# Kernel optimization log

Measured on AMD Instinct MI355X. Metric: run time of the kernel, lower is better.

## Reference

```python
import jax, jax.numpy as jnp
import numpy as np

B, S, N, E = 8, 64, 512, 32  # batch, seq_size, node_num, embed_size


def setup_inputs() -> dict:
    key = jax.random.key(0)
    k0, k1, k2, k3, k4 = jax.random.split(key, 5)
    x = jax.random.normal(k0, (B, S, N), dtype=jnp.float32)
    # lin_w: Linear(2*S, E) -> weight (E, 2*S), bias (E,)
    W = jax.random.normal(k1, (E, 2 * S), dtype=jnp.float32) * (1.0 / np.sqrt(2 * S))
    b_w = jax.random.normal(k2, (E,), dtype=jnp.float32) * 0.01
    # lin_a: Linear(E, 1) -> weight (E,), bias scalar
    Wa = jax.random.normal(k3, (E,), dtype=jnp.float32) * (1.0 / np.sqrt(E))
    b_a = jax.random.normal(k4, (), dtype=jnp.float32) * 0.01
    return {"x": x, "W": W, "b_w": b_w, "Wa": Wa, "b_a": b_a}


def reference(x, W, b_w, Wa, b_a):
    # Faithful to MP_GAT.forward in eval mode (dropout = identity).
    # Algebraic decomposition: lin_w(cat(vi, vj)) = vi @ Wi^T + vj @ Wj^T + b,
    # where W = [Wi | Wj] along the input dim -- avoids the O(N^2 * 2S) concat.
    s = W.shape[1] // 2
    v = jnp.transpose(x, (0, 2, 1))          # (B, N, S)
    Wi, Wj = W[:, :s], W[:, s:]              # (E, S) each
    ti = jnp.einsum('bns,es->bne', v, Wi)    # (B, N, E)
    tj = jnp.einsum('bns,es->bne', v, Wj)    # (B, N, E)
    pre = ti[:, :, None, :] + tj[:, None, :, :] + b_w  # (B, N, N, E)
    xw = jnp.where(pre > 0, pre, 0.2 * pre)  # LeakyReLU(0.2)
    e = jnp.einsum('bije,e->bij', xw, Wa) + b_a        # (B, N, N) = lin_a(...).squeeze
    attention = jax.nn.softmax(e, axis=2)
    h = jax.nn.sigmoid(jnp.einsum('bij,bjs->bis', attention, v))  # (B, N, S)
    return jnp.transpose(h, (0, 2, 1)), attention      # (B, S, N), (B, N, N)
```

## Files before the change

kernel.cpp:

```cpp
#include <hip/hip_runtime.h>
#include <math.h>

#define BB 8
#define SS 64
#define NN 512
#define EE 32
#define IT 16

typedef __attribute__((ext_vector_type(8))) short short8v;
typedef __attribute__((ext_vector_type(4))) float f32x4;

__device__ __forceinline__ unsigned short f2bf(float f) {
    union { float f; unsigned u; } v; v.f = f;
    unsigned r = v.u + 0x7fffu + ((v.u >> 16) & 1u);
    return (unsigned short)(r >> 16);
}
__device__ __forceinline__ float bflo(unsigned u) { return __uint_as_float(u << 16); }
__device__ __forceinline__ float bfhi(unsigned u) { return __uint_as_float(u & 0xffff0000u); }
__device__ __forceinline__ unsigned packtr(float lo, float hi) {
    return (__float_as_uint(hi) & 0xffff0000u) | (__float_as_uint(lo) >> 16);
}

__global__ __launch_bounds__(128) void proj_kernel(
    const float* __restrict__ x, const float* __restrict__ W,
    const float* __restrict__ b_w, const float* __restrict__ Wa,
    float* __restrict__ tip, unsigned short* __restrict__ tjb,
    float* __restrict__ cip, float* __restrict__ djp)
{
    __shared__ float sW[SS][65];
    const int t = threadIdx.x;
    const int wg = ((blockIdx.x & 7) << 6) | (blockIdx.x >> 3);
    const int b = wg >> 6;
    const int n0 = (wg & 63) << 3;

#pragma unroll
    for (int r = 0; r < 8; ++r) {
        int idx = r * 512 + t * 4;
        float4 w4 = *(const float4*)(W + idx);
        int e = idx >> 7;
        int sp = idx & 127;
        int eo = ((sp >> 6) << 5) | e;
        int s0 = sp & 63;
        sW[s0 + 0][eo] = w4.x;
        sW[s0 + 1][eo] = w4.y;
        sW[s0 + 2][eo] = w4.z;
        sW[s0 + 3][eo] = w4.w;
    }
    __syncthreads();

    const int eo = t & 63;
    const int ng = t >> 6;
    const float* xb = x + (size_t)b * SS * NN + n0 + (ng << 2);
    float a0 = 0.f, a1 = 0.f, a2 = 0.f, a3 = 0.f;
#pragma unroll 8
    for (int s = 0; s < SS; ++s) {
        float wv = sW[s][eo];
        float4 xv = *(const float4*)(xb + (size_t)s * NN);
        a0 = fmaf(wv, xv.x, a0);
        a1 = fmaf(wv, xv.y, a1);
        a2 = fmaf(wv, xv.z, a2);
        a3 = fmaf(wv, xv.w, a3);
    }
    const int e = eo & 31;
    const bool isI = eo < EE;
    if (isI) {
        float bias = b_w[e];
        a0 += bias; a1 += bias; a2 += bias; a3 += bias;
        *(float4*)(tip + ((size_t)(b * EE + e)) * NN + n0 + (ng << 2)) =
            make_float4(a0, a1, a2, a3);
    } else {
        unsigned u0 = f2bf(a0) | ((unsigned)f2bf(a1) << 16);
        unsigned u1 = f2bf(a2) | ((unsigned)f2bf(a3) << 16);
        *(uint2*)(tjb + ((size_t)(b * EE + e)) * NN + n0 + (ng << 2)) =
            make_uint2(u0, u1);
    }

    float wa = Wa[e];
    float r0 = wa * a0, r1 = wa * a1, r2 = wa * a2, r3 = wa * a3;
#pragma unroll
    for (int off = 1; off <= 16; off <<= 1) {
        r0 += __shfl_xor(r0, off);
        r1 += __shfl_xor(r1, off);
        r2 += __shfl_xor(r2, off);
        r3 += __shfl_xor(r3, off);
    }
    if (eo == 0)
        *(float4*)(cip + (size_t)b * NN + n0 + (ng << 2)) = make_float4(r0, r1, r2, r3);
    if (eo == 32)
        *(float4*)(djp + (size_t)b * NN + n0 + (ng << 2)) = make_float4(r0, r1, r2, r3);
}

__global__ __launch_bounds__(512) void attn_kernel(
    const float* __restrict__ x,
    const float* __restrict__ tip,
    const unsigned short* __restrict__ tjb,
    const float* __restrict__ cip,
    const float* __restrict__ djp,
    const float* __restrict__ Wa,
    float* __restrict__ out0,
    float* __restrict__ out1)
{
    __shared__ __align__(16) unsigned short stj[EE * NN];
    __shared__ __align__(16) unsigned short prT[IT * 520];
    __shared__ __align__(16) float s_tiT[IT][36];
    __shared__ __align__(16) float hp[2][SS][17];
    __shared__ __align__(16) float red[8][IT];
    __shared__ float s_inv[IT];

    const int t = threadIdx.x;
    const int wg = ((blockIdx.x & 7) << 5) | (blockIdx.x >> 3);
    const int b = wg >> 5;
    const int i0 = (wg & 31) << 4;
    const int lane = t & 63;
    const int w = t >> 6;

    {
        int i = t & 15, e = t >> 4;
        s_tiT[i][e] = tip[((size_t)(b * EE + e)) * NN + i0 + i];
    }
    {
        const uint4* src = (const uint4*)(tjb + (size_t)b * EE * NN);
        uint4* dst = (uint4*)stj;
#pragma unroll
        for (int r = 0; r < 4; ++r) dst[r * 512 + t] = src[r * 512 + t];
    }
    __syncthreads();

    const int ip = t & 7;
    const int jc = t >> 3;
    const int j0 = jc << 3;
    const int ia = 2 * ip, ib2 = 2 * ip + 1;

    float rti0[EE], rti1[EE];
#pragma unroll
    for (int q = 0; q < 8; ++q) {
        float4 v = *(const float4*)&s_tiT[ia][q << 2];
        rti0[4 * q + 0] = v.x; rti0[4 * q + 1] = v.y;
        rti0[4 * q + 2] = v.z; rti0[4 * q + 3] = v.w;
        float4 u = *(const float4*)&s_tiT[ib2][q << 2];
        rti1[4 * q + 0] = u.x; rti1[4 * q + 1] = u.y;
        rti1[4 * q + 2] = u.z; rti1[4 * q + 3] = u.w;
    }

    float acc0[8], acc1[8];
#pragma unroll
    for (int k = 0; k < 8; ++k) { acc0[k] = 0.f; acc1[k] = 0.f; }

#pragma unroll
    for (int e = 0; e < EE; ++e) {
        uint4 d = *(const uint4*)&stj[e * NN + j0];
        float wa = Wa[e];
        float t0 = rti0[e], t1 = rti1[e];
        float tjf[8];
        tjf[0] = bflo(d.x); tjf[1] = bfhi(d.x);
        tjf[2] = bflo(d.y); tjf[3] = bfhi(d.y);
        tjf[4] = bflo(d.z); tjf[5] = bfhi(d.z);
        tjf[6] = bflo(d.w); tjf[7] = bfhi(d.w);
#pragma unroll
        for (int k = 0; k < 8; ++k) {
            acc0[k] = fmaf(fabsf(t0 + tjf[k]), wa, acc0[k]);
            acc1[k] = fmaf(fabsf(t1 + tjf[k]), wa, acc1[k]);
        }
    }

    float dj8[8];
    {
        float4 d0 = *(const float4*)(djp + (size_t)b * NN + j0);
        float4 d1 = *(const float4*)(djp + (size_t)b * NN + j0 + 4);
        dj8[0] = d0.x; dj8[1] = d0.y; dj8[2] = d0.z; dj8[3] = d0.w;
        dj8[4] = d1.x; dj8[5] = d1.y; dj8[6] = d1.z; dj8[7] = d1.w;
    }
    float c0 = cip[(size_t)b * NN + i0 + ia];
    float c1 = cip[(size_t)b * NN + i0 + ib2];
    float pr0[8], pr1[8];
#pragma unroll
    for (int k = 0; k < 8; ++k) {
        pr0[k] = __expf(fmaf(0.4f, acc0[k], 0.6f * (c0 + dj8[k])));
        pr1[k] = __expf(fmaf(0.4f, acc1[k], 0.6f * (c1 + dj8[k])));
    }

    {
        uint4 pa, pb;
        pa.x = f2bf(pr0[0]) | ((unsigned)f2bf(pr0[1]) << 16);
        pa.y = f2bf(pr0[2]) | ((unsigned)f2bf(pr0[3]) << 16);
        pa.z = f2bf(pr0[4]) | ((unsigned)f2bf(pr0[5]) << 16);
        pa.w = f2bf(pr0[6]) | ((unsigned)f2bf(pr0[7]) << 16);
        pb.x = f2bf(pr1[0]) | ((unsigned)f2bf(pr1[1]) << 16);
        pb.y = f2bf(pr1[2]) | ((unsigned)f2bf(pr1[3]) << 16);
        pb.z = f2bf(pr1[4]) | ((unsigned)f2bf(pr1[5]) << 16);
        pb.w = f2bf(pr1[6]) | ((unsigned)f2bf(pr1[7]) << 16);
        *(uint4*)&prT[ia * 520 + j0]  = pa;
        *(uint4*)&prT[ib2 * 520 + j0] = pb;
    }

    float rs0 = 0.f, rs1 = 0.f;
#pragma unroll
    for (int k = 0; k < 8; ++k) { rs0 += pr0[k]; rs1 += pr1[k]; }
#pragma unroll
    for (int off = 8; off <= 32; off <<= 1) {
        rs0 += __shfl_xor(rs0, off);
        rs1 += __shfl_xor(rs1, off);
    }
    if (lane < 8) { red[w][2 * lane] = rs0; red[w][2 * lane + 1] = rs1; }
    __syncthreads();
    if (t < IT) {
        float S = 0.f;
#pragma unroll
        for (int ww = 0; ww < 8; ++ww) S += red[ww][t];
        s_inv[t] = 1.0f / S;
    }
    __syncthreads();

    {
        float v0 = s_inv[ia], v1 = s_inv[ib2];
        float* r0p = out1 + ((size_t)(b * NN + i0 + ia)) * NN + j0;
        float* r1p = out1 + ((size_t)(b * NN + i0 + ib2)) * NN + j0;
        *(float4*)(r0p)     = make_float4(pr0[0]*v0, pr0[1]*v0, pr0[2]*v0, pr0[3]*v0);
        *(float4*)(r0p + 4) = make_float4(pr0[4]*v0, pr0[5]*v0, pr0[6]*v0, pr0[7]*v0);
        *(float4*)(r1p)     = make_float4(pr1[0]*v1, pr1[1]*v1, pr1[2]*v1, pr1[3]*v1);
        *(float4*)(r1p + 4) = make_float4(pr1[4]*v1, pr1[5]*v1, pr1[6]*v1, pr1[7]*v1);
    }

    {
        const int mt = w & 3;
        const int kh = w >> 2;
        const int lm = lane & 15;
        const int ko = lane >> 4;
        const float* xrow = x + ((size_t)(b * SS + mt * 16 + lm)) * NN;

        f32x4 acc = {0.f, 0.f, 0.f, 0.f};
#pragma unroll
        for (int st = 0; st < 8; ++st) {
            const int j = kh * 256 + st * 32 + ko * 8;
            float4 xa = *(const float4*)(xrow + j);
            float4 xb2 = *(const float4*)(xrow + j + 4);
            union { unsigned u[4]; short8v v; } af;
            af.u[0] = packtr(xa.x, xa.y);
            af.u[1] = packtr(xa.z, xa.w);
            af.u[2] = packtr(xb2.x, xb2.y);
            af.u[3] = packtr(xb2.z, xb2.w);
            short8v bf = *(const short8v*)&prT[lm * 520 + j];
            acc = __builtin_amdgcn_mfma_f32_16x16x32_bf16(af.v, bf, acc, 0, 0, 0);
        }
#pragma unroll
        for (int r = 0; r < 4; ++r) {
            int s = mt * 16 + (lane >> 4) * 4 + r;
            hp[kh][s][lm] = acc[r];
        }
    }
    __syncthreads();

    {
        int i = t & 15, sb = t >> 4;
        float vi = s_inv[i];
#pragma unroll
        for (int rr = 0; rr < 2; ++rr) {
            int s = sb + 32 * rr;
            float h = (hp[0][s][i] + hp[1][s][i]) * vi;
            out0[((size_t)(b * SS + s)) * NN + i0 + i] = 1.0f / (1.0f + __expf(-h));
        }
    }
}

extern "C" void kernel_launch(void* const* d_in, const int* in_sizes, int n_in,
                              void* d_out, int out_size, void* d_ws, size_t ws_size,
                              hipStream_t stream) {
    const float* x   = (const float*)d_in[0];
    const float* W   = (const float*)d_in[1];
    const float* b_w = (const float*)d_in[2];
    const float* Wa  = (const float*)d_in[3];

    float* out0 = (float*)d_out;
    float* out1 = (float*)d_out + (size_t)BB * SS * NN;

    float* tip = (float*)d_ws;
    unsigned short* tjb = (unsigned short*)(tip + (size_t)BB * EE * NN);
    float* cip = (float*)(tjb + (size_t)BB * EE * NN);
    float* djp = cip + (size_t)BB * NN;

    proj_kernel<<<BB * (NN / 8), 128, 0, stream>>>(x, W, b_w, Wa, tip, tjb, cip, djp);
    attn_kernel<<<BB * (NN / IT), 512, 0, stream>>>(x, tip, tjb, cip, djp, Wa, out0, out1);
}
```

Measured before the change: 20.40 us.

## Fuse projection and attention kernels with per-batch atomic grid barrier

Merges the projection kernel into the attention kernel. Each workgroup computes its own 16 nodes' ti/ci into shared memory and writes its tj/dj slice to global memory. A per-batch atomic counter spin-wait then makes all 32 workgroups of a batch wait until the batch's full tj is available. This removes one kernel launch and the global round trip for ti/ci. In exchange it adds a memset launch and depends on all 32 workgroups of a batch being co-resident to avoid deadlock, with 256 workgroups of 512 threads spinning.

Result: slower. 39.74 us (+94.8%).

```diff
diff --git a/kernel.cpp b/kernel.cpp
--- a/kernel.cpp
+++ b/kernel.cpp
@@ -21,21 +21,33 @@
     return (__float_as_uint(hi) & 0xffff0000u) | (__float_as_uint(lo) >> 16);
 }
 
-__global__ __launch_bounds__(128) void proj_kernel(
+__global__ __launch_bounds__(512) void fused_kernel(
     const float* __restrict__ x, const float* __restrict__ W,
     const float* __restrict__ b_w, const float* __restrict__ Wa,
-    float* __restrict__ tip, unsigned short* __restrict__ tjb,
-    float* __restrict__ cip, float* __restrict__ djp)
+    unsigned short* __restrict__ tjb,
+    float* __restrict__ djp,
+    int* __restrict__ cnt,
+    float* __restrict__ out0, float* __restrict__ out1)
 {
-    __shared__ float sW[SS][65];
+    __shared__ __align__(16) unsigned short stj[EE * NN];
+    __shared__ __align__(16) float sW[SS][65];
+    __shared__ __align__(16) unsigned short prT[IT * 520];
+    __shared__ __align__(16) float s_tiT[IT][36];
+    __shared__ __align__(16) float hp[2][SS][17];
+    __shared__ __align__(16) float red[8][IT];
+    __shared__ float s_inv[IT];
+    __shared__ float s_ci[IT];
+
     const int t = threadIdx.x;
-    const int wg = ((blockIdx.x & 7) << 6) | (blockIdx.x >> 3);
-    const int b = wg >> 6;
-    const int n0 = (wg & 63) << 3;
-
-#pragma unroll
-    for (int r = 0; r < 8; ++r) {
-        int idx = r * 512 + t * 4;
+    const int wg = ((blockIdx.x & 7) << 5) | (blockIdx.x >> 3);
+    const int b = wg >> 5;
+    const int i0 = (wg & 31) << 4;
+    const int lane = t & 63;
+    const int w = t >> 6;
+
+#pragma unroll
+    for (int r = 0; r < 2; ++r) {
+        int idx = r * 2048 + t * 4;
         float4 w4 = *(const float4*)(W + idx);
         int e = idx >> 7;
         int sp = idx & 127;
@@ -48,76 +60,51 @@
     }
     __syncthreads();
 
-    const int eo = t & 63;
-    const int ng = t >> 6;
-    const float* xb = x + (size_t)b * SS * NN + n0 + (ng << 2);
-    float a0 = 0.f, a1 = 0.f, a2 = 0.f, a3 = 0.f;
+    {
+        const int eo = t & 63;
+        const int np = t >> 6;
+        const float* xb = x + (size_t)b * SS * NN + i0 + np * 2;
+        float a0 = 0.f, a1 = 0.f;
 #pragma unroll 8
-    for (int s = 0; s < SS; ++s) {
-        float wv = sW[s][eo];
-        float4 xv = *(const float4*)(xb + (size_t)s * NN);
-        a0 = fmaf(wv, xv.x, a0);
-        a1 = fmaf(wv, xv.y, a1);
-        a2 = fmaf(wv, xv.z, a2);
-        a3 = fmaf(wv, xv.w, a3);
-    }
-    const int e = eo & 31;
-    const bool isI = eo < EE;
-    if (isI) {
-        float bias = b_w[e];
-        a0 += bias; a1 += bias; a2 += bias; a3 += bias;
-        *(float4*)(tip + ((size_t)(b * EE + e)) * NN + n0 + (ng << 2)) =
-            make_float4(a0, a1, a2, a3);
-    } else {
-        unsigned u0 = f2bf(a0) | ((unsigned)f2bf(a1) << 16);
-        unsigned u1 = f2bf(a2) | ((unsigned)f2bf(a3) << 16);
-        *(uint2*)(tjb + ((size_t)(b * EE + e)) * NN + n0 + (ng << 2)) =
-            make_uint2(u0, u1);
-    }
-
-    float wa = Wa[e];
-    float r0 = wa * a0, r1 = wa * a1, r2 = wa * a2, r3 = wa * a3;
-#pragma unroll
-    for (int off = 1; off <= 16; off <<= 1) {
-        r0 += __shfl_xor(r0, off);
-        r1 += __shfl_xor(r1, off);
-        r2 += __shfl_xor(r2, off);
-        r3 += __shfl_xor(r3, off);
-    }
-    if (eo == 0)
-        *(float4*)(cip + (size_t)b * NN + n0 + (ng << 2)) = make_float4(r0, r1, r2, r3);
-    if (eo == 32)
-        *(float4*)(djp + (size_t)b * NN + n0 + (ng << 2)) = make_float4(r0, r1, r2, r3);
-}
-
-__global__ __launch_bounds__(512) void attn_kernel(
-    const float* __restrict__ x,
-    const float* __restrict__ tip,
-    const unsigned short* __restrict__ tjb,
-    const float* __restrict__ cip,
-    const float* __restrict__ djp,
-    const float* __restrict__ Wa,
-    float* __restrict__ out0,
-    float* __restrict__ out1)
-{
-    __shared__ __align__(16) unsigned short stj[EE * NN];
-    __shared__ __align__(16) unsigned short prT[IT * 520];
-    __shared__ __align__(16) float s_tiT[IT][36];
-    __shared__ __align__(16) float hp[2][SS][17];
-    __shared__ __align__(16) float red[8][IT];
-    __shared__ float s_inv[IT];
-
-    const int t = threadIdx.x;
-    const int wg = ((blockIdx.x & 7) << 5) | (blockIdx.x >> 3);
-    const int b = wg >> 5;
-    const int i0 = (wg & 31) << 4;
-    const int lane = t & 63;
-    const int w = t >> 6;
-
-    {
-        int i = t & 15, e = t >> 4;
-        s_tiT[i][e] = tip[((size_t)(b * EE + e)) * NN + i0 + i];
-    }
+        for (int s = 0; s < SS; ++s) {
+            float wv = sW[s][eo];
+            float2 xv = *(const float2*)(xb + (size_t)s * NN);
+            a0 = fmaf(wv, xv.x, a0);
+            a1 = fmaf(wv, xv.y, a1);
+        }
+        const int e = eo & 31;
+        if (eo < EE) {
+            float bias = b_w[e];
+            a0 += bias; a1 += bias;
+            s_tiT[np * 2 + 0][e] = a0;
+            s_tiT[np * 2 + 1][e] = a1;
+        } else {
+            *(unsigned*)&tjb[((size_t)(b * EE + e)) * NN + i0 + np * 2] =
+                f2bf(a0) | ((unsigned)f2bf(a1) << 16);
+        }
+        float wa = Wa[e];
+        float r0 = wa * a0, r1 = wa * a1;
+#pragma unroll
+        for (int off = 1; off <= 16; off <<= 1) {
+            r0 += __shfl_xor(r0, off);
+            r1 += __shfl_xor(r1, off);
+        }
+        if (eo == 0) { s_ci[np * 2] = r0; s_ci[np * 2 + 1] = r1; }
+        if (eo == 32)
+            *(float2*)(djp + (size_t)b * NN + i0 + np * 2) = make_float2(r0, r1);
+    }
+
+    __syncthreads();
+    if (t == 0) {
+        __threadfence();
+        atomicAdd(&cnt[b], 1);
+        while (__hip_atomic_load(&cnt[b], __ATOMIC_ACQUIRE,
+                                 __HIP_MEMORY_SCOPE_AGENT) < 32) {
+            __builtin_amdgcn_s_sleep(2);
+        }
+    }
+    __syncthreads();
+
     {
         const uint4* src = (const uint4*)(tjb + (size_t)b * EE * NN);
         uint4* dst = (uint4*)stj;
@@ -170,8 +157,8 @@
         dj8[0] = d0.x; dj8[1] = d0.y; dj8[2] = d0.z; dj8[3] = d0.w;
         dj8[4] = d1.x; dj8[5] = d1.y; dj8[6] = d1.z; dj8[7] = d1.w;
     }
-    float c0 = cip[(size_t)b * NN + i0 + ia];
-    float c1 = cip[(size_t)b * NN + i0 + ib2];
+    float c0 = s_ci[ia];
+    float c1 = s_ci[ib2];
     float pr0[8], pr1[8];
 #pragma unroll
     for (int k = 0; k < 8; ++k) {
@@ -273,11 +260,11 @@
     float* out0 = (float*)d_out;
     float* out1 = (float*)d_out + (size_t)BB * SS * NN;
 
-    float* tip = (float*)d_ws;
-    unsigned short* tjb = (unsigned short*)(tip + (size_t)BB * EE * NN);
-    float* cip = (float*)(tjb + (size_t)BB * EE * NN);
-    float* djp = cip + (size_t)BB * NN;
-
-    proj_kernel<<<BB * (NN / 8), 128, 0, stream>>>(x, W, b_w, Wa, tip, tjb, cip, djp);
-    attn_kernel<<<BB * (NN / IT), 512, 0, stream>>>(x, tip, tjb, cip, djp, Wa, out0, out1);
-}
+    unsigned short* tjb = (unsigned short*)d_ws;
+    float* djp = (float*)(tjb + (size_t)BB * EE * NN);
+    int* cnt = (int*)(djp + (size_t)BB * NN);
+
+    hipMemsetAsync(cnt, 0, BB * sizeof(int), stream);
+    fused_kernel<<<BB * (NN / IT), 512, 0, stream>>>(
+        x, W, b_w, Wa, tjb, djp, cnt, out0, out1);
+}
```
